# Kernel tuning notes

Measured on AMD Instinct MI355X. Metric: run time of the kernel, lower is better.

Reference implementation:

```python
import jax, jax.numpy as jnp
import numpy as np

NUM_POINTS = 1_000_000
WINDOW = 8                      # 2^3 corner stencil for linear shape functions in 3D
GRID = (128, 128, 128)
NUM_CELLS = GRID[0] * GRID[1] * GRID[2]
CELL = 1.0 / 64.0
INV_CELL = 64.0
ORIGIN = jnp.zeros((3,), dtype=jnp.float32)
# forward_window: the 8 corner offsets of the enclosing cell
FWD_WINDOW = jnp.array([[i, j, k] for i in (0, 1) for j in (0, 1) for k in (0, 1)],
                       dtype=jnp.int32)  # [8,3]


def setup_inputs() -> dict:
    key = jax.random.key(0)
    k1, k2, k3 = jax.random.split(key, 3)
    domain = GRID[0] * CELL
    # keep particles one cell away from the boundary so all stencil hashes are in range
    pos = jax.random.uniform(k1, (NUM_POINTS, 3), dtype=jnp.float32) * (domain - 2 * CELL) + CELL
    vel = jax.random.normal(k2, (NUM_POINTS, 3), dtype=jnp.float32)
    mass = jax.random.uniform(k3, (NUM_POINTS,), dtype=jnp.float32) * 1e-3 + 1e-4
    return {"position_stack": pos, "velocity_stack": vel, "mass_stack": mass}


def reference(position_stack, velocity_stack, mass_stack):
    # ---- get_interactions: gather particle pos, hash into grid, shape functions ----
    rel = (position_stack - ORIGIN) * INV_CELL               # [N,3] position in cell units
    base = jnp.floor(rel)                                    # [N,3]
    grid_pos = base[:, None, :] + FWD_WINDOW[None, :, :].astype(rel.dtype)  # [N,8,3]
    dist = rel[:, None, :] - grid_pos                        # [N,8,3], each dim in (-1,1)

    gp = grid_pos.astype(jnp.int32)
    # get_hash, dim==3: pos[2] + pos[0]*grid[2] + pos[1]*grid[2]*grid[0]
    intr_hash = gp[..., 2] + gp[..., 0] * GRID[2] + gp[..., 1] * (GRID[2] * GRID[0])  # [N,8]

    # linear shape function: N = prod_d (1 - |x_d|); grad scaled by inv_cell_size
    w = 1.0 - jnp.abs(dist)                                  # [N,8,3]
    shapef = w[..., 0] * w[..., 1] * w[..., 2]               # [N,8]
    valid = (intr_hash >= 0) & (intr_hash < NUM_CELLS)
    shapef = jnp.where(valid, shapef, 0.0)

    g0 = -jnp.sign(dist[..., 0]) * w[..., 1] * w[..., 2]
    g1 = -jnp.sign(dist[..., 1]) * w[..., 0] * w[..., 2]
    g2 = -jnp.sign(dist[..., 2]) * w[..., 0] * w[..., 1]
    shapef_grad = jnp.stack([g0, g1, g2], axis=-1) * INV_CELL  # [N,8,3]
    shapef_grad = jnp.where(valid[..., None], shapef_grad, 0.0)

    # intr_dist_padded = -dist * cell_size (kept implicitly via dist; used in APIC-style p2g)
    # ---- p2g scatter (vmap_intr_scatter semantics): mass & momentum to grid nodes ----
    h_flat = jnp.clip(intr_hash, 0, NUM_CELLS - 1).reshape(-1)  # [N*8]
    sm = shapef * mass_stack[:, None]                           # [N,8]
    node_mass = jax.ops.segment_sum(sm.reshape(-1), h_flat, num_segments=NUM_CELLS)   # [C]
    mom = sm[..., None] * velocity_stack[:, None, :]            # [N,8,3]
    node_mom = jax.ops.segment_sum(mom.reshape(-1, 3), h_flat, num_segments=NUM_CELLS)  # [C,3]

    return jnp.concatenate([node_mass[:, None], node_mom], axis=1)  # [C,4]
```

## Files before the change

kernel.cpp:

```cpp
#include <hip/hip_runtime.h>
#include <hip/hip_fp16.h>


#define GRID_DIM   128
#define NUM_CELLS  (GRID_DIM * GRID_DIM * GRID_DIM)
#define INV_CELL   64.0f
#define OVF_MAX    65536
#define SCAN_BLKS  2048

#define NREG       512
#define RCAP       2560
#define PPB        4096
#define MAXCAP     3
#define NSEG       27
#define NREC       2369
#define EPAD(sc)   ((sc) * 3 + ((sc) >> 2))

typedef float floatx4 __attribute__((ext_vector_type(4)));

__device__ __forceinline__ int cell_id(int ix, int iy, int iz) {
    return iz + ix * GRID_DIM + iy * (GRID_DIM * GRID_DIM);
}

__device__ __forceinline__ unsigned int q16(float f) {
    int q = (int)(f * 65536.0f + 0.5f);
    return (unsigned int)min(q, 65535);
}
__device__ __forceinline__ unsigned int f2h(float f) {
    return (unsigned int)__half_as_ushort(__float2half(f));
}
__device__ __forceinline__ float h2f(unsigned int b) {
    return __half2float(__ushort_as_half((unsigned short)(b & 0xffffu)));
}

__global__ __launch_bounds__(1024) void region_bin_kernel(
    const float* __restrict__ pos, const float* __restrict__ vel,
    const float* __restrict__ mass, unsigned int* __restrict__ region_cursor,
    uint4* __restrict__ regbuf, int* __restrict__ ovf_cnt,
    uint4* __restrict__ ovf_rec, unsigned int* __restrict__ ovf_reg, int n)
{
    __shared__ uint4 rec_lds[PPB];
    __shared__ unsigned short regof[PPB];
    __shared__ unsigned int cnt[NREG];
    __shared__ unsigned int lofs[NREG];
    __shared__ unsigned int gbase[NREG];
    __shared__ unsigned int wtot[8];

    int tid = threadIdx.x;
    int base_i = blockIdx.x * PPB;
    int blockn = min(PPB, n - base_i);

    if (tid < NREG) cnt[tid] = 0;
    __syncthreads();

    uint4 r_[4]; int reg_[4], rank_[4], val_[4];
    #pragma unroll
    for (int k = 0; k < 4; ++k) {
        int e = k * 1024 + tid;
        int i = base_i + e;
        val_[k] = (e < blockn);
        reg_[k] = 0; rank_[k] = 0;
        if (val_[k]) {
            float px = __builtin_nontemporal_load(&pos[3 * i + 0]);
            float py = __builtin_nontemporal_load(&pos[3 * i + 1]);
            float pz = __builtin_nontemporal_load(&pos[3 * i + 2]);
            float rx = px * INV_CELL, ry = py * INV_CELL, rz = pz * INV_CELL;
            float bx = floorf(rx), by = floorf(ry), bz = floorf(rz);
            float fx = rx - bx, fy = ry - by, fz = rz - bz;
            int ix = min(max((int)bx, 0), GRID_DIM - 1);
            int iy = min(max((int)by, 0), GRID_DIM - 1);
            int iz = min(max((int)bz, 0), GRID_DIM - 1);
            int reg = (iz >> 4) | ((ix >> 4) << 3) | ((iy >> 4) << 6);
            unsigned int cid = (unsigned int)((iz & 15) | ((ix & 15) << 4)
                                                        | ((iy & 15) << 8));
            float m  = __builtin_nontemporal_load(&mass[i]);
            float vx = __builtin_nontemporal_load(&vel[3 * i + 0]);
            float vy = __builtin_nontemporal_load(&vel[3 * i + 1]);
            float vz = __builtin_nontemporal_load(&vel[3 * i + 2]);
            uint4 r;
            r.x = q16(fx) | (q16(fy) << 16);
            r.y = q16(fz) | (f2h(m) << 16);
            r.z = f2h(vx) | (f2h(vy) << 16);
            r.w = f2h(vz) | (cid << 16);
            r_[k] = r;
            reg_[k] = reg;
            rank_[k] = (int)atomicAdd(&cnt[reg], 1u);
        }
    }
    __syncthreads();

    unsigned int c = 0, v = 0;
    if (tid < NREG) {
        c = cnt[tid];
        v = c;
        #pragma unroll
        for (int d = 1; d < 64; d <<= 1) {
            unsigned int t = __shfl_up(v, d, 64);
            if ((tid & 63) >= d) v += t;
        }
        if ((tid & 63) == 63) wtot[tid >> 6] = v;
    }
    __syncthreads();
    if (tid == 0) {
        unsigned int run = 0;
        #pragma unroll
        for (int w = 0; w < 8; ++w) { unsigned int t = wtot[w]; wtot[w] = run; run += t; }
    }
    __syncthreads();
    if (tid < NREG) {
        lofs[tid] = wtot[tid >> 6] + v - c;
        if (c) gbase[tid] = atomicAdd(&region_cursor[tid], c);
    }
    __syncthreads();

    #pragma unroll
    for (int k = 0; k < 4; ++k) {
        if (val_[k]) {
            int d = (int)lofs[reg_[k]] + rank_[k];
            rec_lds[d] = r_[k];
            regof[d] = (unsigned short)reg_[k];
        }
    }
    __syncthreads();

    for (int e = tid; e < blockn; e += 1024) {
        uint4 rr = rec_lds[e];
        int rg = (int)regof[e];
        unsigned int slot = gbase[rg] + (unsigned int)(e - (int)lofs[rg]);
        if (slot < (unsigned int)RCAP) {
            regbuf[(size_t)rg * RCAP + slot] = rr;
        } else {
            int o = atomicAdd(ovf_cnt, 1);
            if (o < OVF_MAX) { ovf_rec[o] = rr; ovf_reg[o] = (unsigned int)rg; }
        }
    }
}

__global__ __launch_bounds__(1024) void tile_sort_kernel(
    uint4* __restrict__ regbuf, const unsigned int* __restrict__ region_cursor,
    unsigned int* __restrict__ tile_off)
{
    __shared__ uint4 out_lds[RCAP];
    __shared__ unsigned int cnt64[64];
    __shared__ unsigned int tofs[65];

    int r = blockIdx.x;
    int tid = threadIdx.x;
    int cntR = (int)min(region_cursor[r], (unsigned int)RCAP);

    if (tid < 64) cnt64[tid] = 0;
    __syncthreads();

    uint4 rr_[3]; int t_[3], rk_[3], vl_[3];
    #pragma unroll
    for (int k = 0; k < 3; ++k) {
        int e = k * 1024 + tid;
        vl_[k] = (e < cntR);
        t_[k] = 0; rk_[k] = 0;
        if (vl_[k]) {
            uint4 rr = regbuf[(size_t)r * RCAP + e];
            unsigned int cid = rr.w >> 16;
            int t = (int)(((cid & 15u) >> 2) | ((((cid >> 4) & 15u) >> 2) << 2)
                                             | ((((cid >> 8) & 15u) >> 2) << 4));
            rr_[k] = rr;
            t_[k] = t;
            rk_[k] = (int)atomicAdd(&cnt64[t], 1u);
        }
    }
    __syncthreads();

    if (tid < 64) {
        unsigned int c = cnt64[tid], v = c;
        #pragma unroll
        for (int d = 1; d < 64; d <<= 1) {
            unsigned int t = __shfl_up(v, d, 64);
            if (tid >= d) v += t;
        }
        tofs[tid] = v - c;
        if (tid == 63) tofs[64] = v;
    }
    __syncthreads();

    #pragma unroll
    for (int k = 0; k < 3; ++k)
        if (vl_[k]) out_lds[(int)tofs[t_[k]] + rk_[k]] = rr_[k];
    __syncthreads();

    for (int e = tid; e < cntR; e += 1024)
        regbuf[(size_t)r * RCAP + e] = out_lds[e];
    if (tid < 65) tile_off[r * 65 + tid] = tofs[tid];
}

__global__ __launch_bounds__(512) void tile_gather2_kernel(
    const uint4* __restrict__ regbuf, const unsigned int* __restrict__ tile_off,
    float4* __restrict__ out)
{
    __shared__ float4 recA[NREC];
    __shared__ unsigned int recB[NREC];
    __shared__ unsigned int cnt_s[729];
    __shared__ unsigned int seg_gb[NSEG];
    __shared__ unsigned short seg_reg[NSEG];
    __shared__ unsigned int seg_off[NSEG + 1];
    __shared__ int ovf_n;
    __shared__ short ovf_sc[64];
    __shared__ uint4 ovf_rec[64];

    int tid = threadIdx.x;
    int swz = (blockIdx.x & 7) * 512 + (blockIdx.x >> 3);
    int bz = swz & 15;
    int bx = (swz >> 4) & 15;
    int by = swz >> 8;
    int g0x = bx * 8, g0y = by * 8, g0z = bz * 8;
    int Tz0 = bz * 2 - 1, Tx0 = bx * 2 - 1, Ty0 = by * 2 - 1;

    for (int s2 = tid; s2 < 729; s2 += 512) cnt_s[s2] = 0;
    if (tid == 0) ovf_n = 0;

    if (tid < 64) {
        unsigned int c = 0;
        if (tid < NSEG) {
            int ltz = tid % 3, q = tid / 3, ltx = q % 3, lty = q / 3;
            int Tz = Tz0 + ltz, Tx = Tx0 + ltx, Ty = Ty0 + lty;
            unsigned int gb = 0; int reg = 0;
            if ((Tz >= 0) & (Tx >= 0) & (Ty >= 0)) {
                reg = (Tz >> 2) | ((Tx >> 2) << 3) | ((Ty >> 2) << 6);
                int tl = (Tz & 3) | ((Tx & 3) << 2) | ((Ty & 3) << 4);
                unsigned int o0 = tile_off[reg * 65 + tl];
                unsigned int o1 = tile_off[reg * 65 + tl + 1];
                c = o1 - o0;
                gb = (unsigned int)reg * RCAP + o0;
            }
            seg_reg[tid] = (unsigned short)reg;
            seg_gb[tid] = gb;
        }
        unsigned int v = c;
        #pragma unroll
        for (int d = 1; d < 64; d <<= 1) {
            unsigned int t = __shfl_up(v, d, 64);
            if (tid >= d) v += t;
        }
        if (tid < NSEG) seg_off[tid] = v - c;
        if (tid == NSEG - 1) seg_off[NSEG] = v;
    }
    __syncthreads();
    int R = (int)seg_off[NSEG];

    for (int r = tid; r < R; r += 512) {
        int s = 0;
        #pragma unroll
        for (int step = 16; step >= 1; step >>= 1)
            if (s + step <= NSEG && (int)seg_off[s + step] <= r) s += step;
        int j = r - (int)seg_off[s];
        uint4 rec = regbuf[seg_gb[s] + j];
        unsigned int cid = rec.w >> 16;
        int reg = (int)seg_reg[s];
        int cz = (reg & 7) * 16 + (int)(cid & 15u);
        int cx = ((reg >> 3) & 7) * 16 + (int)((cid >> 4) & 15u);
        int cy = ((reg >> 6) & 7) * 16 + (int)((cid >> 8) & 15u);
        int uz = cz - (g0z - 1), ux = cx - (g0x - 1), uy = cy - (g0y - 1);
        if (((unsigned)uz < 9u) & ((unsigned)ux < 9u) & ((unsigned)uy < 9u)) {
            int sc = uy * 81 + ux * 9 + uz;
            unsigned int j2 = atomicAdd(&cnt_s[sc], 1u);
            if (j2 < MAXCAP) {
                int e = EPAD(sc) + (int)j2;
                float fx = (float)(rec.x & 0xffffu) * (1.0f / 65536.0f);
                float fy = (float)(rec.x >> 16)     * (1.0f / 65536.0f);
                float fz = (float)(rec.y & 0xffffu) * (1.0f / 65536.0f);
                recA[e] = make_float4(fx, fy, fz, __uint_as_float(rec.z));
                recB[e] = (rec.y >> 16) | (rec.w << 16);
            } else {
                int o = atomicAdd(&ovf_n, 1);
                if (o < 64) { ovf_sc[o] = (short)sc; ovf_rec[o] = rec; }
            }
        }
    }
    __syncthreads();

    int tz = tid & 7, tx = (tid >> 3) & 7, ty = tid >> 6;
    float a0 = 0.0f, a1 = 0.0f, a2 = 0.0f, a3 = 0.0f;

    #pragma unroll
    for (int dy = 0; dy < 2; ++dy) {
        #pragma unroll
        for (int dx = 0; dx < 2; ++dx) {
            int scb = (ty + dy) * 81 + (tx + dx) * 9 + tz;
            #pragma unroll
            for (int dz = 0; dz < 2; ++dz) {
                int sc = scb + dz;
                int cnt = min((int)cnt_s[sc], MAXCAP);
                int eb = EPAD(sc);
                for (int j = 0; j < cnt; ++j) {
                    float4 A = recA[eb + j];
                    unsigned int B = recB[eb + j];
                    unsigned int w3 = __float_as_uint(A.w);
                    float wx = dx ? (1.0f - A.x) : A.x;
                    float wy = dy ? (1.0f - A.y) : A.y;
                    float wz = dz ? (1.0f - A.z) : A.z;
                    float sm = wx * wy * wz * h2f(B);
                    a0 += sm;
                    a1 += sm * h2f(w3);
                    a2 += sm * h2f(w3 >> 16);
                    a3 += sm * h2f(B >> 16);
                }
            }
        }
    }

    int no = min(ovf_n, 64);
    for (int e2 = 0; e2 < no; ++e2) {
        int sc = (int)ovf_sc[e2];
        int uzv = sc % 9, t2 = sc / 9, uxv = t2 % 9, uyv = t2 / 9;
        int ddz = uzv - tz, ddx = uxv - tx, ddy = uyv - ty;
        if (((unsigned)ddz < 2u) & ((unsigned)ddx < 2u) & ((unsigned)ddy < 2u)) {
            uint4 rec = ovf_rec[e2];
            float fx = (float)(rec.x & 0xffffu) * (1.0f / 65536.0f);
            float fy = (float)(rec.x >> 16)     * (1.0f / 65536.0f);
            float fz = (float)(rec.y & 0xffffu) * (1.0f / 65536.0f);
            float wx = ddx ? (1.0f - fx) : fx;
            float wy = ddy ? (1.0f - fy) : fy;
            float wz = ddz ? (1.0f - fz) : fz;
            float sm = wx * wy * wz * h2f(rec.y >> 16);
            a0 += sm;
            a1 += sm * h2f(rec.z);
            a2 += sm * h2f(rec.z >> 16);
            a3 += sm * h2f(rec.w);
        }
    }

    int id = (g0z + tz) + (g0x + tx) * GRID_DIM
           + (g0y + ty) * (GRID_DIM * GRID_DIM);
    floatx4 vv = { a0, a1, a2, a3 };
    __builtin_nontemporal_store(vv, (floatx4*)&out[id]);
}

__global__ __launch_bounds__(256) void fixup_packed_kernel(
    const int* __restrict__ ovf_cnt, const uint4* __restrict__ ovf_rec,
    const unsigned int* __restrict__ ovf_reg, float* __restrict__ out)
{
    int total = min(*ovf_cnt, OVF_MAX);
    for (int k = blockIdx.x * 256 + threadIdx.x; k < total; k += gridDim.x * 256) {
        uint4 rec = ovf_rec[k];
        unsigned int reg = ovf_reg[k];
        unsigned int cid = rec.w >> 16;
        int iz = (int)(reg & 7u) * 16 + (int)(cid & 15u);
        int ix = (int)((reg >> 3) & 7u) * 16 + (int)((cid >> 4) & 15u);
        int iy = (int)((reg >> 6) & 7u) * 16 + (int)((cid >> 8) & 15u);
        float fx = (float)(rec.x & 0xffffu) * (1.0f / 65536.0f);
        float fy = (float)(rec.x >> 16)     * (1.0f / 65536.0f);
        float fz = (float)(rec.y & 0xffffu) * (1.0f / 65536.0f);
        float m  = h2f(rec.y >> 16);
        float vx = h2f(rec.z), vy = h2f(rec.z >> 16), vz = h2f(rec.w);
        float wx[2] = { 1.0f - fx, fx }, wy[2] = { 1.0f - fy, fy }, wz[2] = { 1.0f - fz, fz };
        #pragma unroll
        for (int a = 0; a < 2; ++a)
            #pragma unroll
            for (int b = 0; b < 2; ++b)
                #pragma unroll
                for (int c = 0; c < 2; ++c) {
                    int h = cell_id(ix + a, iy + b, iz + c);
                    bool valid = (h >= 0) && (h < NUM_CELLS);
                    int hc = min(max(h, 0), NUM_CELLS - 1);
                    float s = valid ? (wx[a] * wy[b] * wz[c]) : 0.0f;
                    float sm = s * m;
                    float* cell = out + 4 * (size_t)hc;
                    atomicAdd(cell + 0, sm);
                    atomicAdd(cell + 1, sm * vx);
                    atomicAdd(cell + 2, sm * vy);
                    atomicAdd(cell + 3, sm * vz);
                }
    }
}

__global__ __launch_bounds__(256) void s_hist_kernel(
    const float* __restrict__ pos, int* __restrict__ counts, int n)
{
    int i = blockIdx.x * 256 + threadIdx.x;
    if (i >= n) return;
    int ix = min(max((int)floorf(pos[3 * i + 0] * INV_CELL), 0), GRID_DIM - 1);
    int iy = min(max((int)floorf(pos[3 * i + 1] * INV_CELL), 0), GRID_DIM - 1);
    int iz = min(max((int)floorf(pos[3 * i + 2] * INV_CELL), 0), GRID_DIM - 1);
    atomicAdd(&counts[cell_id(ix, iy, iz)], 1);
}

__global__ __launch_bounds__(256) void s_scan_partials_kernel(
    const int* __restrict__ counts, int* __restrict__ partials)
{
    __shared__ int red[256];
    int t = threadIdx.x;
    int4 v = ((const int4*)counts)[blockIdx.x * 256 + t];
    red[t] = v.x + v.y + v.z + v.w;
    __syncthreads();
    for (int off = 128; off > 0; off >>= 1) {
        if (t < off) red[t] += red[t + off];
        __syncthreads();
    }
    if (t == 0) partials[blockIdx.x] = red[0];
}

__global__ __launch_bounds__(1024) void s_scan_tops_kernel(int* __restrict__ partials)
{
    __shared__ int s[1024];
    int t = threadIdx.x;
    int p0 = partials[2 * t], p1 = partials[2 * t + 1];
    int sum = p0 + p1;
    s[t] = sum;
    __syncthreads();
    for (int off = 1; off < 1024; off <<= 1) {
        int x = (t >= off) ? s[t - off] : 0;
        __syncthreads();
        s[t] += x;
        __syncthreads();
    }
    int excl = s[t] - sum;
    partials[2 * t] = excl;
    partials[2 * t + 1] = excl + p0;
}

__global__ __launch_bounds__(256) void s_scan_final_kernel(
    const int* __restrict__ counts, const int* __restrict__ partials,
    int* __restrict__ offsets, int* __restrict__ cursors)
{
    __shared__ int s[256];
    int t = threadIdx.x;
    int g = blockIdx.x * 256 + t;
    int4 v = ((const int4*)counts)[g];
    int sum = v.x + v.y + v.z + v.w;
    s[t] = sum;
    __syncthreads();
    for (int off = 1; off < 256; off <<= 1) {
        int x = (t >= off) ? s[t - off] : 0;
        __syncthreads();
        s[t] += x;
        __syncthreads();
    }
    int run = partials[blockIdx.x] + s[t] - sum;
    int4 o = make_int4(run, run + v.x, run + v.x + v.y, run + v.x + v.y + v.z);
    ((int4*)offsets)[g] = o;
    ((int4*)cursors)[g] = o;
}

__global__ __launch_bounds__(256) void s_binplace_kernel(
    const float* __restrict__ pos, const float* __restrict__ vel,
    const float* __restrict__ mass, int* __restrict__ cursors,
    float4* __restrict__ records, int n)
{
    int i = blockIdx.x * 256 + threadIdx.x;
    if (i >= n) return;
    float rx = pos[3 * i + 0] * INV_CELL;
    float ry = pos[3 * i + 1] * INV_CELL;
    float rz = pos[3 * i + 2] * INV_CELL;
    int ix = min(max((int)floorf(rx), 0), GRID_DIM - 1);
    int iy = min(max((int)floorf(ry), 0), GRID_DIM - 1);
    int iz = min(max((int)floorf(rz), 0), GRID_DIM - 1);
    int slot = atomicAdd(&cursors[cell_id(ix, iy, iz)], 1);
    records[2 * slot + 0] = make_float4(rx, ry, rz, mass[i]);
    records[2 * slot + 1] = make_float4(vel[3 * i + 0], vel[3 * i + 1],
                                        vel[3 * i + 2], 0.0f);
}

__global__ __launch_bounds__(256) void s_node_gather_kernel(
    const float4* __restrict__ records, const int* __restrict__ offsets,
    const int* __restrict__ cursors, float4* __restrict__ out)
{
    int id = blockIdx.x * 256 + threadIdx.x;
    int gz = id & (GRID_DIM - 1);
    int gx = (id >> 7) & (GRID_DIM - 1);
    int gy = id >> 14;
    float fgx = (float)gx, fgy = (float)gy, fgz = (float)gz;
    float a0 = 0.0f, a1 = 0.0f, a2 = 0.0f, a3 = 0.0f;
    int z0 = max(gz - 1, 0), y0 = max(gy - 1, 0), x0 = max(gx - 1, 0);
    for (int cy = y0; cy <= gy; ++cy) {
        for (int cx = x0; cx <= gx; ++cx) {
            int cb = cx * GRID_DIM + cy * (GRID_DIM * GRID_DIM);
            int beg = offsets[cb + z0];
            int end = cursors[cb + gz];
            for (int p = beg; p < end; ++p) {
                float4 r0 = records[2 * p + 0];
                float4 r1 = records[2 * p + 1];
                float w = (1.0f - fabsf(r0.x - fgx)) *
                          (1.0f - fabsf(r0.y - fgy)) *
                          (1.0f - fabsf(r0.z - fgz));
                float sm = w * r0.w;
                a0 += sm; a1 += sm * r1.x; a2 += sm * r1.y; a3 += sm * r1.z;
            }
        }
    }
    out[id] = make_float4(a0, a1, a2, a3);
}

__global__ __launch_bounds__(256) void p2g_scatter_kernel(
    const float* __restrict__ pos, const float* __restrict__ vel,
    const float* __restrict__ mass, float* __restrict__ out, int n)
{
    int i = blockIdx.x * blockDim.x + threadIdx.x;
    if (i >= n) return;
    float px = pos[3 * i + 0] * INV_CELL;
    float py = pos[3 * i + 1] * INV_CELL;
    float pz = pos[3 * i + 2] * INV_CELL;
    float bx = floorf(px), by = floorf(py), bz = floorf(pz);
    float fx = px - bx, fy = py - by, fz = pz - bz;
    int ix = (int)bx, iy = (int)by, iz = (int)bz;
    float m = mass[i];
    float vx = vel[3 * i + 0], vy = vel[3 * i + 1], vz = vel[3 * i + 2];
    float wx[2] = { 1.0f - fx, fx }, wy[2] = { 1.0f - fy, fy }, wz[2] = { 1.0f - fz, fz };
    #pragma unroll
    for (int a = 0; a < 2; ++a)
        #pragma unroll
        for (int b = 0; b < 2; ++b)
            #pragma unroll
            for (int c = 0; c < 2; ++c) {
                int h = cell_id(ix + a, iy + b, iz + c);
                bool valid = (h >= 0) && (h < NUM_CELLS);
                int hc = min(max(h, 0), NUM_CELLS - 1);
                float s = valid ? (wx[a] * wy[b] * wz[c]) : 0.0f;
                float sm = s * m;
                float* cell = out + 4 * (size_t)hc;
                atomicAdd(cell + 0, sm);
                atomicAdd(cell + 1, sm * vx);
                atomicAdd(cell + 2, sm * vy);
                atomicAdd(cell + 3, sm * vz);
            }
}

extern "C" void kernel_launch(void* const* d_in, const int* in_sizes, int n_in,
                              void* d_out, int out_size, void* d_ws, size_t ws_size,
                              hipStream_t stream) {
    const float* pos  = (const float*)d_in[0];
    const float* vel  = (const float*)d_in[1];
    const float* mass = (const float*)d_in[2];
    float* out = (float*)d_out;
    int n = in_sizes[2];
    int blocks = (n + 255) / 256;

    size_t w_off_tileoff = 4096;
    size_t w_off_ovfcnt  = w_off_tileoff + (size_t)NREG * 65 * 4;
    size_t w_off_ovfrec  = w_off_ovfcnt + 256;
    size_t w_off_ovfreg  = w_off_ovfrec + (size_t)OVF_MAX * 16;
    size_t w_off_regbuf  = w_off_ovfreg + (size_t)OVF_MAX * 4;
    size_t need_twopass  = w_off_regbuf + (size_t)NREG * RCAP * 16;

    size_t s_off_offsets  = (size_t)NUM_CELLS * 4;
    size_t s_off_records  = s_off_offsets + (size_t)NUM_CELLS * 4;
    size_t s_off_partials = s_off_records + (size_t)n * 32;
    size_t need_sorted    = s_off_partials + (size_t)SCAN_BLKS * 4;

    if (ws_size >= need_twopass) {
        char* ws = (char*)d_ws;
        unsigned int* region_cursor = (unsigned int*)ws;
        unsigned int* tile_off = (unsigned int*)(ws + w_off_tileoff);
        int* ovf_cnt           = (int*)(ws + w_off_ovfcnt);
        uint4* ovf_rec         = (uint4*)(ws + w_off_ovfrec);
        unsigned int* ovf_reg  = (unsigned int*)(ws + w_off_ovfreg);
        uint4* regbuf          = (uint4*)(ws + w_off_regbuf);

        (void)hipMemsetAsync(region_cursor, 0, (size_t)NREG * 4, stream);
        (void)hipMemsetAsync(ovf_cnt, 0, 4, stream);
        region_bin_kernel<<<(n + PPB - 1) / PPB, 1024, 0, stream>>>(
            pos, vel, mass, region_cursor, regbuf, ovf_cnt, ovf_rec, ovf_reg, n);
        tile_sort_kernel<<<NREG, 1024, 0, stream>>>(regbuf, region_cursor,
                                                    tile_off);
        tile_gather2_kernel<<<4096, 512, 0, stream>>>(regbuf, tile_off,
                                                      (float4*)out);
        fixup_packed_kernel<<<16, 256, 0, stream>>>(ovf_cnt, ovf_rec,
                                                    ovf_reg, out);
    } else if (ws_size >= need_sorted) {
        char* ws = (char*)d_ws;
        int* counts   = (int*)ws;
        int* offsets  = (int*)(ws + s_off_offsets);
        float4* records = (float4*)(ws + s_off_records);
        int* partials = (int*)(ws + s_off_partials);

        (void)hipMemsetAsync(counts, 0, (size_t)NUM_CELLS * 4, stream);
        s_hist_kernel<<<blocks, 256, 0, stream>>>(pos, counts, n);
        s_scan_partials_kernel<<<SCAN_BLKS, 256, 0, stream>>>(counts, partials);
        s_scan_tops_kernel<<<1, 1024, 0, stream>>>(partials);
        s_scan_final_kernel<<<SCAN_BLKS, 256, 0, stream>>>(counts, partials,
                                                           offsets, counts);
        s_binplace_kernel<<<blocks, 256, 0, stream>>>(pos, vel, mass, counts,
                                                      records, n);
        s_node_gather_kernel<<<NUM_CELLS / 256, 256, 0, stream>>>(
            records, offsets, counts, (float4*)out);
    } else {
        (void)hipMemsetAsync(out, 0, (size_t)out_size * sizeof(float), stream);
        p2g_scatter_kernel<<<blocks, 256, 0, stream>>>(pos, vel, mass, out, n);
    }
}
```

Measured before the change: 163.5 us.

## Sort records per cell and gather nodes directly from global cell ranges

The region sort now buckets records by full 4096-cell key instead of 64 tiles and writes per-cell offsets. The node gather kernel drops its LDS staging of a 9x9x9 neighbourhood, along with its capped slots and in-block overflow. Instead, each node thread reads its 8 neighbouring cells' record ranges straight from global memory. This removes the shared-memory staging pass and its synchronisation, but adds a larger offset table, more scattered global loads per thread, and a bigger LDS histogram and scan in the sort.

```diff
diff --git a/kernel.cpp b/kernel.cpp
--- a/kernel.cpp
+++ b/kernel.cpp
@@ -11,10 +11,6 @@
 #define NREG       512
 #define RCAP       2560
 #define PPB        4096
-#define MAXCAP     3
-#define NSEG       27
-#define NREC       2369
-#define EPAD(sc)   ((sc) * 3 + ((sc) >> 2))
 
 typedef float floatx4 __attribute__((ext_vector_type(4)));
 
@@ -136,199 +132,120 @@
     }
 }
 
-__global__ __launch_bounds__(1024) void tile_sort_kernel(
+__global__ __launch_bounds__(1024) void cell_sort_kernel(
     uint4* __restrict__ regbuf, const unsigned int* __restrict__ region_cursor,
-    unsigned int* __restrict__ tile_off)
+    unsigned int* __restrict__ cell_off)
 {
     __shared__ uint4 out_lds[RCAP];
-    __shared__ unsigned int cnt64[64];
-    __shared__ unsigned int tofs[65];
+    __shared__ unsigned int cnt[4096];
+    __shared__ unsigned int wsum[16];
 
     int r = blockIdx.x;
     int tid = threadIdx.x;
     int cntR = (int)min(region_cursor[r], (unsigned int)RCAP);
 
-    if (tid < 64) cnt64[tid] = 0;
-    __syncthreads();
-
-    uint4 rr_[3]; int t_[3], rk_[3], vl_[3];
+    for (int c = tid; c < 4096; c += 1024) cnt[c] = 0;
+    __syncthreads();
+
+    uint4 rr_[3]; int cid_[3], rk_[3], vl_[3];
     #pragma unroll
     for (int k = 0; k < 3; ++k) {
         int e = k * 1024 + tid;
         vl_[k] = (e < cntR);
-        t_[k] = 0; rk_[k] = 0;
+        cid_[k] = 0; rk_[k] = 0;
         if (vl_[k]) {
             uint4 rr = regbuf[(size_t)r * RCAP + e];
-            unsigned int cid = rr.w >> 16;
-            int t = (int)(((cid & 15u) >> 2) | ((((cid >> 4) & 15u) >> 2) << 2)
-                                             | ((((cid >> 8) & 15u) >> 2) << 4));
+            int cid = (int)((rr.w >> 16) & 4095u);
             rr_[k] = rr;
-            t_[k] = t;
-            rk_[k] = (int)atomicAdd(&cnt64[t], 1u);
-        }
-    }
-    __syncthreads();
-
-    if (tid < 64) {
-        unsigned int c = cnt64[tid], v = c;
+            cid_[k] = cid;
+            rk_[k] = (int)atomicAdd(&cnt[cid], 1u);
+        }
+    }
+    __syncthreads();
+
+    unsigned int s0 = cnt[4 * tid + 0], s1 = cnt[4 * tid + 1];
+    unsigned int s2 = cnt[4 * tid + 2], s3 = cnt[4 * tid + 3];
+    unsigned int tsum = s0 + s1 + s2 + s3;
+    unsigned int v = tsum;
+    #pragma unroll
+    for (int d = 1; d < 64; d <<= 1) {
+        unsigned int t = __shfl_up(v, d, 64);
+        if ((tid & 63) >= d) v += t;
+    }
+    if ((tid & 63) == 63) wsum[tid >> 6] = v;
+    __syncthreads();
+    if (tid == 0) {
+        unsigned int run = 0;
         #pragma unroll
-        for (int d = 1; d < 64; d <<= 1) {
-            unsigned int t = __shfl_up(v, d, 64);
-            if (tid >= d) v += t;
-        }
-        tofs[tid] = v - c;
-        if (tid == 63) tofs[64] = v;
-    }
+        for (int w = 0; w < 16; ++w) { unsigned int t = wsum[w]; wsum[w] = run; run += t; }
+    }
+    __syncthreads();
+    unsigned int base = wsum[tid >> 6] + v - tsum;
+    cnt[4 * tid + 0] = base;
+    cnt[4 * tid + 1] = base + s0;
+    cnt[4 * tid + 2] = base + s0 + s1;
+    cnt[4 * tid + 3] = base + s0 + s1 + s2;
     __syncthreads();
 
     #pragma unroll
     for (int k = 0; k < 3; ++k)
-        if (vl_[k]) out_lds[(int)tofs[t_[k]] + rk_[k]] = rr_[k];
+        if (vl_[k]) out_lds[(int)cnt[cid_[k]] + rk_[k]] = rr_[k];
     __syncthreads();
 
     for (int e = tid; e < cntR; e += 1024)
         regbuf[(size_t)r * RCAP + e] = out_lds[e];
-    if (tid < 65) tile_off[r * 65 + tid] = tofs[tid];
-}
-
-__global__ __launch_bounds__(512) void tile_gather2_kernel(
-    const uint4* __restrict__ regbuf, const unsigned int* __restrict__ tile_off,
+    for (int c = tid; c < 4096; c += 1024)
+        cell_off[(size_t)r * 4097 + c] = cnt[c];
+    if (tid == 0) cell_off[(size_t)r * 4097 + 4096] = (unsigned int)cntR;
+}
+
+__global__ __launch_bounds__(512) void node_gather_kernel(
+    const uint4* __restrict__ regbuf, const unsigned int* __restrict__ cell_off,
     float4* __restrict__ out)
 {
-    __shared__ float4 recA[NREC];
-    __shared__ unsigned int recB[NREC];
-    __shared__ unsigned int cnt_s[729];
-    __shared__ unsigned int seg_gb[NSEG];
-    __shared__ unsigned short seg_reg[NSEG];
-    __shared__ unsigned int seg_off[NSEG + 1];
-    __shared__ int ovf_n;
-    __shared__ short ovf_sc[64];
-    __shared__ uint4 ovf_rec[64];
-
     int tid = threadIdx.x;
     int swz = (blockIdx.x & 7) * 512 + (blockIdx.x >> 3);
     int bz = swz & 15;
     int bx = (swz >> 4) & 15;
     int by = swz >> 8;
-    int g0x = bx * 8, g0y = by * 8, g0z = bz * 8;
-    int Tz0 = bz * 2 - 1, Tx0 = bx * 2 - 1, Ty0 = by * 2 - 1;
-
-    for (int s2 = tid; s2 < 729; s2 += 512) cnt_s[s2] = 0;
-    if (tid == 0) ovf_n = 0;
-
-    if (tid < 64) {
-        unsigned int c = 0;
-        if (tid < NSEG) {
-            int ltz = tid % 3, q = tid / 3, ltx = q % 3, lty = q / 3;
-            int Tz = Tz0 + ltz, Tx = Tx0 + ltx, Ty = Ty0 + lty;
-            unsigned int gb = 0; int reg = 0;
-            if ((Tz >= 0) & (Tx >= 0) & (Ty >= 0)) {
-                reg = (Tz >> 2) | ((Tx >> 2) << 3) | ((Ty >> 2) << 6);
-                int tl = (Tz & 3) | ((Tx & 3) << 2) | ((Ty & 3) << 4);
-                unsigned int o0 = tile_off[reg * 65 + tl];
-                unsigned int o1 = tile_off[reg * 65 + tl + 1];
-                c = o1 - o0;
-                gb = (unsigned int)reg * RCAP + o0;
-            }
-            seg_reg[tid] = (unsigned short)reg;
-            seg_gb[tid] = gb;
-        }
-        unsigned int v = c;
-        #pragma unroll
-        for (int d = 1; d < 64; d <<= 1) {
-            unsigned int t = __shfl_up(v, d, 64);
-            if (tid >= d) v += t;
-        }
-        if (tid < NSEG) seg_off[tid] = v - c;
-        if (tid == NSEG - 1) seg_off[NSEG] = v;
-    }
-    __syncthreads();
-    int R = (int)seg_off[NSEG];
-
-    for (int r = tid; r < R; r += 512) {
-        int s = 0;
-        #pragma unroll
-        for (int step = 16; step >= 1; step >>= 1)
-            if (s + step <= NSEG && (int)seg_off[s + step] <= r) s += step;
-        int j = r - (int)seg_off[s];
-        uint4 rec = regbuf[seg_gb[s] + j];
-        unsigned int cid = rec.w >> 16;
-        int reg = (int)seg_reg[s];
-        int cz = (reg & 7) * 16 + (int)(cid & 15u);
-        int cx = ((reg >> 3) & 7) * 16 + (int)((cid >> 4) & 15u);
-        int cy = ((reg >> 6) & 7) * 16 + (int)((cid >> 8) & 15u);
-        int uz = cz - (g0z - 1), ux = cx - (g0x - 1), uy = cy - (g0y - 1);
-        if (((unsigned)uz < 9u) & ((unsigned)ux < 9u) & ((unsigned)uy < 9u)) {
-            int sc = uy * 81 + ux * 9 + uz;
-            unsigned int j2 = atomicAdd(&cnt_s[sc], 1u);
-            if (j2 < MAXCAP) {
-                int e = EPAD(sc) + (int)j2;
+    int tz = tid & 7, tx = (tid >> 3) & 7, ty = tid >> 6;
+    int gz = bz * 8 + tz, gx = bx * 8 + tx, gy = by * 8 + ty;
+
+    float a0 = 0.0f, a1 = 0.0f, a2 = 0.0f, a3 = 0.0f;
+
+    #pragma unroll
+    for (int dy = 0; dy < 2; ++dy)
+    #pragma unroll
+    for (int dx = 0; dx < 2; ++dx)
+    #pragma unroll
+    for (int dz = 0; dz < 2; ++dz) {
+        int cz = gz - 1 + dz, cx = gx - 1 + dx, cy = gy - 1 + dy;
+        if (((unsigned)cz < (unsigned)GRID_DIM) &
+            ((unsigned)cx < (unsigned)GRID_DIM) &
+            ((unsigned)cy < (unsigned)GRID_DIM)) {
+            int reg = (cz >> 4) | ((cx >> 4) << 3) | ((cy >> 4) << 6);
+            int cid = (cz & 15) | ((cx & 15) << 4) | ((cy & 15) << 8);
+            const unsigned int* co = cell_off + (size_t)reg * 4097 + cid;
+            unsigned int o0 = co[0], o1 = co[1];
+            const uint4* bp = regbuf + (size_t)reg * RCAP;
+            for (unsigned int j = o0; j < o1; ++j) {
+                uint4 rec = bp[j];
                 float fx = (float)(rec.x & 0xffffu) * (1.0f / 65536.0f);
                 float fy = (float)(rec.x >> 16)     * (1.0f / 65536.0f);
                 float fz = (float)(rec.y & 0xffffu) * (1.0f / 65536.0f);
-                recA[e] = make_float4(fx, fy, fz, __uint_as_float(rec.z));
-                recB[e] = (rec.y >> 16) | (rec.w << 16);
-            } else {
-                int o = atomicAdd(&ovf_n, 1);
-                if (o < 64) { ovf_sc[o] = (short)sc; ovf_rec[o] = rec; }
+                float wxv = dx ? (1.0f - fx) : fx;
+                float wyv = dy ? (1.0f - fy) : fy;
+                float wzv = dz ? (1.0f - fz) : fz;
+                float sm = wxv * wyv * wzv * h2f(rec.y >> 16);
+                a0 += sm;
+                a1 += sm * h2f(rec.z);
+                a2 += sm * h2f(rec.z >> 16);
+                a3 += sm * h2f(rec.w);
             }
         }
     }
-    __syncthreads();
-
-    int tz = tid & 7, tx = (tid >> 3) & 7, ty = tid >> 6;
-    float a0 = 0.0f, a1 = 0.0f, a2 = 0.0f, a3 = 0.0f;
-
-    #pragma unroll
-    for (int dy = 0; dy < 2; ++dy) {
-        #pragma unroll
-        for (int dx = 0; dx < 2; ++dx) {
-            int scb = (ty + dy) * 81 + (tx + dx) * 9 + tz;
-            #pragma unroll
-            for (int dz = 0; dz < 2; ++dz) {
-                int sc = scb + dz;
-                int cnt = min((int)cnt_s[sc], MAXCAP);
-                int eb = EPAD(sc);
-                for (int j = 0; j < cnt; ++j) {
-                    float4 A = recA[eb + j];
-                    unsigned int B = recB[eb + j];
-                    unsigned int w3 = __float_as_uint(A.w);
-                    float wx = dx ? (1.0f - A.x) : A.x;
-                    float wy = dy ? (1.0f - A.y) : A.y;
-                    float wz = dz ? (1.0f - A.z) : A.z;
-                    float sm = wx * wy * wz * h2f(B);
-                    a0 += sm;
-                    a1 += sm * h2f(w3);
-                    a2 += sm * h2f(w3 >> 16);
-                    a3 += sm * h2f(B >> 16);
-                }
-            }
-        }
-    }
-
-    int no = min(ovf_n, 64);
-    for (int e2 = 0; e2 < no; ++e2) {
-        int sc = (int)ovf_sc[e2];
-        int uzv = sc % 9, t2 = sc / 9, uxv = t2 % 9, uyv = t2 / 9;
-        int ddz = uzv - tz, ddx = uxv - tx, ddy = uyv - ty;
-        if (((unsigned)ddz < 2u) & ((unsigned)ddx < 2u) & ((unsigned)ddy < 2u)) {
-            uint4 rec = ovf_rec[e2];
-            float fx = (float)(rec.x & 0xffffu) * (1.0f / 65536.0f);
-            float fy = (float)(rec.x >> 16)     * (1.0f / 65536.0f);
-            float fz = (float)(rec.y & 0xffffu) * (1.0f / 65536.0f);
-            float wx = ddx ? (1.0f - fx) : fx;
-            float wy = ddy ? (1.0f - fy) : fy;
-            float wz = ddz ? (1.0f - fz) : fz;
-            float sm = wx * wy * wz * h2f(rec.y >> 16);
-            a0 += sm;
-            a1 += sm * h2f(rec.z);
-            a2 += sm * h2f(rec.z >> 16);
-            a3 += sm * h2f(rec.w);
-        }
-    }
-
-    int id = (g0z + tz) + (g0x + tx) * GRID_DIM
-           + (g0y + ty) * (GRID_DIM * GRID_DIM);
+
+    int id = gz + gx * GRID_DIM + gy * (GRID_DIM * GRID_DIM);
     floatx4 vv = { a0, a1, a2, a3 };
     __builtin_nontemporal_store(vv, (floatx4*)&out[id]);
 }
@@ -341,7 +258,7 @@
     for (int k = blockIdx.x * 256 + threadIdx.x; k < total; k += gridDim.x * 256) {
         uint4 rec = ovf_rec[k];
         unsigned int reg = ovf_reg[k];
-        unsigned int cid = rec.w >> 16;
+        unsigned int cid = (rec.w >> 16) & 4095u;
         int iz = (int)(reg & 7u) * 16 + (int)(cid & 15u);
         int ix = (int)((reg >> 3) & 7u) * 16 + (int)((cid >> 4) & 15u);
         int iy = (int)((reg >> 6) & 7u) * 16 + (int)((cid >> 8) & 15u);
@@ -532,8 +449,8 @@
     int n = in_sizes[2];
     int blocks = (n + 255) / 256;
 
-    size_t w_off_tileoff = 4096;
-    size_t w_off_ovfcnt  = w_off_tileoff + (size_t)NREG * 65 * 4;
+    size_t w_off_celloff = 4096;
+    size_t w_off_ovfcnt  = w_off_celloff + (size_t)NREG * 4097 * 4;
     size_t w_off_ovfrec  = w_off_ovfcnt + 256;
     size_t w_off_ovfreg  = w_off_ovfrec + (size_t)OVF_MAX * 16;
     size_t w_off_regbuf  = w_off_ovfreg + (size_t)OVF_MAX * 4;
@@ -547,7 +464,7 @@
     if (ws_size >= need_twopass) {
         char* ws = (char*)d_ws;
         unsigned int* region_cursor = (unsigned int*)ws;
-        unsigned int* tile_off = (unsigned int*)(ws + w_off_tileoff);
+        unsigned int* cell_off = (unsigned int*)(ws + w_off_celloff);
         int* ovf_cnt           = (int*)(ws + w_off_ovfcnt);
         uint4* ovf_rec         = (uint4*)(ws + w_off_ovfrec);
         unsigned int* ovf_reg  = (unsigned int*)(ws + w_off_ovfreg);
@@ -557,10 +474,10 @@
         (void)hipMemsetAsync(ovf_cnt, 0, 4, stream);
         region_bin_kernel<<<(n + PPB - 1) / PPB, 1024, 0, stream>>>(
             pos, vel, mass, region_cursor, regbuf, ovf_cnt, ovf_rec, ovf_reg, n);
-        tile_sort_kernel<<<NREG, 1024, 0, stream>>>(regbuf, region_cursor,
-                                                    tile_off);
-        tile_gather2_kernel<<<4096, 512, 0, stream>>>(regbuf, tile_off,
-                                                      (float4*)out);
+        cell_sort_kernel<<<NREG, 1024, 0, stream>>>(regbuf, region_cursor,
+                                                    cell_off);
+        node_gather_kernel<<<4096, 512, 0, stream>>>(regbuf, cell_off,
+                                                     (float4*)out);
         fixup_packed_kernel<<<16, 256, 0, stream>>>(ovf_cnt, ovf_rec,
                                                     ovf_reg, out);
     } else if (ws_size >= need_sorted) {
```

New measurement: 170.8 us. +4.5%, slower.
